# Optimization experiments

Measured on AMD Instinct MI355X. Metric: run time of the kernel, lower is better.

The kernel has to match this reference:

```python
import jax, jax.numpy as jnp
import numpy as np

B, SEQ, NNODES = 4, 12, 1024
SEG_LEN, SEG_NUM = 3, 4
HID, FF, DK, NH, NLAYERS = 64, 2048, 32, 8, 2


def setup_inputs() -> dict:
    key = jax.random.key(0)
    ks = iter(jax.random.split(key, 64))
    def nrm(shape, scale=0.05):
        return jax.random.normal(next(ks), shape, dtype=jnp.float32) * scale
    ones = lambda s: jnp.ones(s, jnp.float32)
    zeros = lambda s: jnp.zeros(s, jnp.float32)
    S, L = 2, NLAYERS
    return {
        'traffic': nrm((B, SEQ, NNODES), 1.0),
        'user': nrm((B, SEQ, NNODES), 1.0),
        'patch_w': nrm((S, HID, SEG_LEN)), 'patch_b': nrm((S, HID)),
        'mha_w': nrm((S, L, 3 * HID, HID)), 'mha_b': nrm((S, L, 3 * HID)),
        'out_w': nrm((S, L, HID, HID)), 'out_b': nrm((S, L, HID)),
        'ff1_w': nrm((S, L, FF, HID)), 'ff1_b': nrm((S, L, FF)),
        'ff2_w': nrm((S, L, HID, FF)), 'ff2_b': nrm((S, L, HID)),
        'ln1_g': ones((S, L, HID)), 'ln1_b': zeros((S, L, HID)),
        'ln2_g': ones((S, L, HID)), 'ln2_b': zeros((S, L, HID)),
        'ga_wq': nrm((S, L, DK, HID)), 'ga_wk': nrm((S, L, DK, HID)), 'ga_wv': nrm((S, L, HID, HID)),
        'ga_ff1_w': nrm((S, L, FF, HID)), 'ga_ff1_b': nrm((S, L, FF)),
        'ga_ff2_w': nrm((S, L, HID, FF)), 'ga_ff2_b': nrm((S, L, HID)),
        'ga_ln1_g': ones((S, L, HID)), 'ga_ln1_b': zeros((S, L, HID)),
        'ga_ln2_g': ones((S, L, HID)), 'ga_ln2_b': zeros((S, L, HID)),
        'ca_wq': nrm((DK, 2 * HID)), 'ca_wk': nrm((DK, 2 * HID)), 'ca_wv': nrm((HID, 2 * HID)),
    }


def _ln(x, g, b, eps=1e-5):
    m = x.mean(-1, keepdims=True)
    v = jnp.mean((x - m) ** 2, -1, keepdims=True)
    return (x - m) / jnp.sqrt(v + eps) * g + b


def _pe(s, d):
    pos = jnp.arange(s, dtype=jnp.float32)[:, None]
    div = jnp.exp(jnp.arange(0, d, 2, dtype=jnp.float32) * (-np.log(10000.0) / d))
    pe = jnp.zeros((s, d), jnp.float32)
    pe = pe.at[:, 0::2].set(jnp.sin(pos * div))
    pe = pe.at[:, 1::2].set(jnp.cos(pos * div))
    return pe


def _mha(x, w, b, wo, bo):
    # standard nn.MultiheadAttention self-attn, batch_first; x: [B,S,H]
    qkv = x @ w.T + b
    q, k, v = jnp.split(qkv, 3, axis=-1)
    def heads(t):
        b_, s_, h_ = t.shape
        return t.reshape(b_, s_, NH, h_ // NH).transpose(0, 2, 1, 3)
    q, k, v = heads(q), heads(k), heads(v)
    scale = 1.0 / jnp.sqrt(jnp.float32(HID // NH))
    att = jax.nn.softmax(jnp.einsum('bhqd,bhkd->bhqk', q, k) * scale, axis=-1)
    o = jnp.einsum('bhqk,bhkd->bhqd', att, v).transpose(0, 2, 1, 3).reshape(x.shape)
    return o @ wo.T + bo


def _enc_layer(x, p):
    # TransformerEncoderLayer_cross, post-norm, dropout=0 (eval)
    x = _ln(x + _mha(x, p['mw'], p['mb'], p['ow'], p['ob']), p['g1'], p['b1'])
    f = jax.nn.relu(x @ p['f1w'].T + p['f1b']) @ p['f2w'].T + p['f2b']
    return _ln(x + f, p['g2'], p['b2'])


def _graph_att(x, p):
    # GraphAttention.forward (bias=None, mask=None, dropout=0)
    q = x @ p['wq'].T
    k = x @ p['wk'].T
    v = x @ p['wv'].T
    dist = jax.nn.softmax(jnp.einsum('bnd,bmd->bnm', q, k) / jnp.sqrt(jnp.float32(DK)), axis=-1)
    att = jnp.einsum('bnm,bmd->bnd', dist, v)
    att = _ln(att, p['g1'], p['b1']) + x
    f = jax.nn.relu(att @ p['f1w'].T + p['f1b']) @ p['f2w'].T + p['f2b']
    return _ln(att + f, p['g2'], p['b2'])


def reference(traffic, user, patch_w, patch_b, mha_w, mha_b, out_w, out_b,
              ff1_w, ff1_b, ff2_w, ff2_b, ln1_g, ln1_b, ln2_g, ln2_b,
              ga_wq, ga_wk, ga_wv, ga_ff1_w, ga_ff1_b, ga_ff2_w, ga_ff2_b,
              ga_ln1_g, ga_ln1_b, ga_ln2_g, ga_ln2_b, ca_wq, ca_wk, ca_wv):
    pe = _pe(SEG_NUM, HID)

    def encode(x, s):
        b, _, d = x.shape
        # DSW_embedding: b (seg_num seg_len) d -> b d seg_num seg_len, then Linear
        seg = x.reshape(b, SEG_NUM, SEG_LEN, d).transpose(0, 3, 1, 2)
        z = seg @ patch_w[s].T + patch_b[s]          # [b, d, seg_num, HID]
        z = z + pe                                    # positional encoding over patches
        for i in range(NLAYERS):
            # temporal attention over the patch axis
            zt = z.reshape(b * d, SEG_NUM, HID)
            zt = _enc_layer(zt, dict(mw=mha_w[s, i], mb=mha_b[s, i], ow=out_w[s, i], ob=out_b[s, i],
                                     f1w=ff1_w[s, i], f1b=ff1_b[s, i], f2w=ff2_w[s, i], f2b=ff2_b[s, i],
                                     g1=ln1_g[s, i], b1=ln1_b[s, i], g2=ln2_g[s, i], b2=ln2_b[s, i]))
            z = zt.reshape(b, d, SEG_NUM, HID)
            # spatial graph attention over the node axis
            zs = z.transpose(0, 2, 1, 3).reshape(b * SEG_NUM, d, HID)
            zs = _graph_att(zs, dict(wq=ga_wq[s, i], wk=ga_wk[s, i], wv=ga_wv[s, i],
                                     f1w=ga_ff1_w[s, i], f1b=ga_ff1_b[s, i], f2w=ga_ff2_w[s, i], f2b=ga_ff2_b[s, i],
                                     g1=ga_ln1_g[s, i], b1=ga_ln1_b[s, i], g2=ga_ln2_g[s, i], b2=ga_ln2_b[s, i]))
            z = zs.reshape(b, SEG_NUM, d, HID).transpose(0, 2, 1, 3)
        return z.mean(axis=2)                         # pool patches -> [b, d, HID]

    enc = jnp.concatenate([encode(traffic, 0), encode(user, 1)], axis=-1)  # [b, d, 2*HID]
    # encoder_attn: SelfAttention(2*HID -> dim_k=32, dim_v=HID)
    q = enc @ ca_wq.T
    k = enc @ ca_wk.T
    v = enc @ ca_wv.T
    dist = jax.nn.softmax(jnp.einsum('bnd,bmd->bnm', q, k) / jnp.sqrt(jnp.float32(DK)), axis=-1)
    return jnp.einsum('bnm,bmd->bnd', dist, v)        # [b, n_nodes, HID]
```

## Files before the change

kernel.cpp:

```cpp
#include <hip/hip_runtime.h>
#include <hip/hip_bf16.h>
#include <math.h>

#define BB 4
#define SEQL 12
#define NN 1024
#define SEGL 3
#define SEGN 4
#define HID 64
#define FFD 2048
#define DKK 32
#define NHH 8
#define HDD 8
#define ZS 1048576

using bf16 = __hip_bfloat16;
__device__ __forceinline__ float b2f(bf16 v) { return __bfloat162float(v); }

typedef __attribute__((ext_vector_type(8))) short s8v;
typedef __attribute__((ext_vector_type(4))) float f4v;
typedef __attribute__((ext_vector_type(4))) unsigned short u4v;

__device__ __forceinline__ unsigned short f2b(float f) {
  bf16 h = __float2bfloat16(f);
  unsigned short u; __builtin_memcpy(&u, &h, 2); return u;
}
__device__ __forceinline__ float us2f(unsigned short u) {
  unsigned int e = ((unsigned int)u) << 16;
  float f; __builtin_memcpy(&f, &e, 4); return f;
}

template <int F>
__device__ __forceinline__ float ldw(const void* p, long i) {
  if (F) return ((const float*)p)[i];
  return b2f(((const bf16*)p)[i]);
}
template <int F>
__device__ __forceinline__ s8v ldfrag(const void* p, long elemOff) {
  if (F) {
    const float* fp = (const float*)p + elemOff;
    f4v u = *(const f4v*)fp, v = *(const f4v*)(fp + 4);
    s8v t;
    t[0]=f2b(u[0]); t[1]=f2b(u[1]); t[2]=f2b(u[2]); t[3]=f2b(u[3]);
    t[4]=f2b(v[0]); t[5]=f2b(v[1]); t[6]=f2b(v[2]); t[7]=f2b(v[3]);
    return t;
  }
  return *(const s8v*)((const unsigned short*)p + elemOff);
}
template <int F>
__device__ __forceinline__ f4v ldb4(const void* p, long i) {
  if (F) return *(const f4v*)((const float*)p + i);
  u4v u = *(const u4v*)((const unsigned short*)p + i);
  f4v r; r[0]=us2f(u[0]); r[1]=us2f(u[1]); r[2]=us2f(u[2]); r[3]=us2f(u[3]);
  return r;
}

__global__ void k_zero(unsigned short* __restrict__ o, int n) {
  int i = blockIdx.x * 256 + threadIdx.x;
  if (i < n) o[i] = 0;
}

__global__ void k_detect(const void* __restrict__ x0, int* __restrict__ flag) {
  int t = threadIdx.x;
  int bad = 0;
  const bf16* p = (const bf16*)x0;
  for (int i = t; i < 512; i += 256) {
    float a = fabsf(b2f(p[i]));
    if (!(a < 1e4f) || (a != 0.f && a < 1e-4f)) bad = 1;
  }
  __shared__ int tot;
  if (t == 0) tot = 0;
  __syncthreads();
  unsigned long long m = __ballot(bad);
  if ((t & 63) == 0) atomicAdd(&tot, __popcll(m));
  __syncthreads();
  if (t == 0) *flag = (tot > 64) ? 1 : 0;
}

template <int F>
__device__ __forceinline__ void wconv_body(const void* __restrict__ w1,
    const void* __restrict__ w2, const void* __restrict__ w3,
    const void* __restrict__ w4, unsigned short* __restrict__ out) {
  int i = blockIdx.x * 256 + threadIdx.x;
  long e8 = (long)i * 8;
  int slot = (int)(e8 >> 17);
  int si = slot >> 2, which = slot & 3;
  long r = e8 & 131071;
  const void* src = (which == 0) ? w1 : (which == 1) ? w2 : (which == 2) ? w3 : w4;
  *(s8v*)(out + e8) = ldfrag<F>(src, (long)si*FFD*HID + r);
}
__global__ __launch_bounds__(256) void k_wconv(const void* w1, const void* w2,
    const void* w3, const void* w4, unsigned short* out,
    const int* __restrict__ flag) {
  if (*flag) wconv_body<1>(w1, w2, w3, w4, out);
  else       wconv_body<0>(w1, w2, w3, w4, out);
}

template <int F>
__device__ __forceinline__ void patch_body(const void* __restrict__ xt,
    const void* __restrict__ xu,
    const void* __restrict__ pw, const void* __restrict__ pb,
    float* __restrict__ z) {
  int bid = blockIdx.x;
  int s = bid >> 12, rem = bid & 4095;
  int b = rem >> 10, n = rem & 1023;
  const void* x = s ? xu : xt;
  long opw = (long)s*HID*SEGL, opb = (long)s*HID;
  int g = threadIdx.x >> 6, h = threadIdx.x & 63;
  float acc = ldw<F>(pb, opb + h);
#pragma unroll
  for (int l = 0; l < SEGL; ++l)
    acc += ldw<F>(x, (long)(b*SEQL + g*SEGL + l)*NN + n) * ldw<F>(pw, opw + h*SEGL + l);
  int i2 = h >> 1;
  float dv = expf((float)(2*i2) * (-logf(10000.f) / (float)HID));
  float ang = (float)g * dv;
  acc += (h & 1) ? cosf(ang) : sinf(ang);
  z[(long)s*ZS + ((long)(b*NN + n)*SEGN + g)*HID + h] = acc;
}
__global__ __launch_bounds__(256) void k_patch(const void* __restrict__ xt,
    const void* __restrict__ xu,
    const void* __restrict__ pw, const void* __restrict__ pb,
    float* __restrict__ z, const int* __restrict__ flag) {
  if (*flag) patch_body<1>(xt, xu, pw, pb, z);
  else       patch_body<0>(xt, xu, pw, pb, z);
}

#define TT 64
template <int F>
__device__ __forceinline__ void tattn_body(float* __restrict__ zb,
    const void* __restrict__ W, const void* __restrict__ bq,
    const void* __restrict__ WO, const void* __restrict__ bo,
    const void* __restrict__ g1, const void* __restrict__ b1,
    int li, char* lds) {
  int s = blockIdx.x >> 8, blk = blockIdx.x & 255;
  long si = s*2 + li;
  float* z = zb + (long)s*ZS;
  long oW = si*3*HID*HID, obq = si*3*HID, oWO = si*HID*HID, obo = si*HID;
  long og1 = si*HID, ob1 = si*HID;
  unsigned short (*qkvs)[200] = (unsigned short(*)[200])lds;
  unsigned short (*ao)[72]    = (unsigned short(*)[72])(lds + 25600);
  float (*yb)[68]             = (float(*)[68])(lds + 34816);
  int tid = threadIdx.x;
  int w = tid >> 6, lane = tid & 63;
  int col = lane & 15, quad = lane >> 4;
  long r0 = (long)blk * TT;

  s8v bx[4][2];
#pragma unroll
  for (int mt = 0; mt < 4; ++mt) {
    const float* xr = z + (r0 + mt*16 + col) * HID;
#pragma unroll
    for (int ks = 0; ks < 2; ++ks) {
      const float* p = xr + ks*32 + quad*8;
      f4v u = *(const f4v*)p, v = *(const f4v*)(p + 4);
      s8v t;
      t[0]=f2b(u[0]); t[1]=f2b(u[1]); t[2]=f2b(u[2]); t[3]=f2b(u[3]);
      t[4]=f2b(v[0]); t[5]=f2b(v[1]); t[6]=f2b(v[2]); t[7]=f2b(v[3]);
      bx[mt][ks] = t;
    }
  }
#pragma unroll
  for (int nt = 0; nt < 3; ++nt) {
    int cbase = (w*3 + nt) * 16;
    s8v aw[2];
#pragma unroll
    for (int ks = 0; ks < 2; ++ks)
      aw[ks] = ldfrag<F>(W, oW + (long)(cbase + col)*HID + ks*32 + quad*8);
    f4v bv = ldb4<F>(bq, obq + cbase + quad*4);
#pragma unroll
    for (int mt = 0; mt < 4; ++mt) {
      f4v sv = (f4v){0.f,0.f,0.f,0.f};
#pragma unroll
      for (int ks = 0; ks < 2; ++ks)
        sv = __builtin_amdgcn_mfma_f32_16x16x32_bf16(aw[ks], bx[mt][ks], sv, 0, 0, 0);
      unsigned short pk[4];
#pragma unroll
      for (int r = 0; r < 4; ++r) pk[r] = f2b(sv[r] + bv[r]);
      *(unsigned long long*)&qkvs[mt*16 + col][cbase + quad*4] =
        (unsigned long long)pk[0] | ((unsigned long long)pk[1] << 16) |
        ((unsigned long long)pk[2] << 32) | ((unsigned long long)pk[3] << 48);
    }
  }
  __syncthreads();
  if (tid < 128) {
    int gi = tid >> 3, hd = tid & 7;
    int tl = gi * 4;
    float qv[4][8], kv[4][8], vv[4][8];
#pragma unroll
    for (int t4 = 0; t4 < 4; ++t4) {
      s8v qq = *(const s8v*)&qkvs[tl + t4][hd*8];
      s8v kk = *(const s8v*)&qkvs[tl + t4][64 + hd*8];
      s8v vq = *(const s8v*)&qkvs[tl + t4][128 + hd*8];
#pragma unroll
      for (int e = 0; e < 8; ++e) {
        qv[t4][e] = us2f((unsigned short)qq[e]);
        kv[t4][e] = us2f((unsigned short)kk[e]);
        vv[t4][e] = us2f((unsigned short)vq[e]);
      }
    }
    const float sc8 = 0.3535533905932738f;
#pragma unroll
    for (int qt = 0; qt < 4; ++qt) {
      float s[4]; float mx = -1e30f;
#pragma unroll
      for (int kt = 0; kt < 4; ++kt) {
        float d = 0;
#pragma unroll
        for (int e = 0; e < 8; ++e) d += qv[qt][e]*kv[kt][e];
        s[kt] = d*sc8; mx = fmaxf(mx, s[kt]);
      }
      float se = 0;
#pragma unroll
      for (int kt = 0; kt < 4; ++kt) { s[kt] = expf(s[kt]-mx); se += s[kt]; }
      float inv = 1.f/se;
      s8v outp;
#pragma unroll
      for (int e = 0; e < 8; ++e) {
        float o = 0;
#pragma unroll
        for (int kt = 0; kt < 4; ++kt) o += s[kt]*vv[kt][e];
        outp[e] = (short)f2b(o*inv);
      }
      *(s8v*)&ao[tl + qt][hd*8] = outp;
    }
  }
  __syncthreads();
  s8v awo[2];
#pragma unroll
  for (int ks = 0; ks < 2; ++ks)
    awo[ks] = ldfrag<F>(WO, oWO + (long)(w*16 + col)*HID + ks*32 + quad*8);
  f4v bov = ldb4<F>(bo, obo + w*16 + quad*4);
#pragma unroll
  for (int mt = 0; mt < 4; ++mt) {
    f4v ov = (f4v){0.f,0.f,0.f,0.f};
#pragma unroll
    for (int ks = 0; ks < 2; ++ks) {
      s8v bao = *(const s8v*)&ao[mt*16 + col][ks*32 + quad*8];
      ov = __builtin_amdgcn_mfma_f32_16x16x32_bf16(awo[ks], bao, ov, 0, 0, 0);
    }
    f4v yv;
#pragma unroll
    for (int r = 0; r < 4; ++r) yv[r] = ov[r] + bov[r];
    *(f4v*)&yb[mt*16 + col][w*16 + quad*4] = yv;
  }
  __syncthreads();
  float gg = ldw<F>(g1, og1 + lane), bb2 = ldw<F>(b1, ob1 + lane);
#pragma unroll
  for (int rr = 0; rr < 16; ++rr) {
    int row = w*16 + rr;
    long tok = r0 + row;
    float val = yb[row][lane] + z[tok*HID + lane];
    float s = val;
#pragma unroll
    for (int off = 32; off; off >>= 1) s += __shfl_xor(s, off);
    float m = s*(1.f/HID);
    float d = val - m, sq = d*d;
#pragma unroll
    for (int off = 32; off; off >>= 1) sq += __shfl_xor(sq, off);
    float rv = rsqrtf(sq*(1.f/HID) + 1e-5f);
    z[tok*HID + lane] = d*rv*gg + bb2;
  }
}
__global__ __launch_bounds__(256) void k_tattn(float* __restrict__ z,
    const void* W, const void* bqkv, const void* WO, const void* bo,
    const void* g1, const void* b1, int li, const int* __restrict__ flag) {
  __shared__ __attribute__((aligned(16))) char lds[52224];
  if (*flag) tattn_body<1>(z, W, bqkv, WO, bo, g1, b1, li, lds);
  else       tattn_body<0>(z, W, bqkv, WO, bo, g1, b1, li, lds);
}

#define FRW 32
#define HCS 74

template <int F>
__device__ __forceinline__ void ffmfma_body(float* __restrict__ xb,
    const unsigned short* __restrict__ wcw, int li, int wsel,
    const void* __restrict__ B1, const void* __restrict__ B2,
    const void* __restrict__ G, const void* __restrict__ Bt,
    char* ldsbuf) {
  int s = blockIdx.x >> 9, blk = blockIdx.x & 511;
  long si = s*2 + li;
  float* x = xb + (long)s*ZS;
  const unsigned short* wc1 = wcw + (si*4 + wsel)*131072;
  const unsigned short* wc2 = wcw + (si*4 + wsel + 1)*131072;
  long ob1 = si*FFD, ob2 = si*HID, og = si*HID, obt = si*HID;
  int tid = threadIdx.x;
  int w = tid >> 6, lane = tid & 63;
  int col = lane & 15, quad = lane >> 4;
  long r0 = (long)blk * FRW;
  unsigned short* hcw = (unsigned short*)(ldsbuf + w*(2*32*HCS));

  s8v bx[2][2];
#pragma unroll
  for (int rt = 0; rt < 2; ++rt) {
    const float* xr = x + (r0 + rt*16 + col) * HID;
#pragma unroll
    for (int ks = 0; ks < 2; ++ks) {
      const float* p = xr + ks*32 + quad*8;
      f4v u = *(const f4v*)p, v = *(const f4v*)(p + 4);
      s8v t;
      t[0]=f2b(u[0]); t[1]=f2b(u[1]); t[2]=f2b(u[2]); t[3]=f2b(u[3]);
      t[4]=f2b(v[0]); t[5]=f2b(v[1]); t[6]=f2b(v[2]); t[7]=f2b(v[3]);
      bx[rt][ks] = t;
    }
  }

  f4v acc[4][2];
#pragma unroll
  for (int m = 0; m < 4; ++m)
#pragma unroll
    for (int rt = 0; rt < 2; ++rt) acc[m][rt] = (f4v){0.f,0.f,0.f,0.f};

  const int hb0 = w * 512;
  for (int c = 0; c < 8; ++c) {
    const int hbase = hb0 + c*64;
#pragma unroll
    for (int t = 0; t < 4; ++t) {
      const unsigned short* a1p = wc1 + (hbase + t*16 + col)*HID + quad*8;
      s8v a10 = *(const s8v*)a1p;
      s8v a11 = *(const s8v*)(a1p + 32);
      f4v bv = ldb4<F>(B1, ob1 + hbase + t*16 + quad*4);
#pragma unroll
      for (int rt = 0; rt < 2; ++rt) {
        f4v sv = __builtin_amdgcn_mfma_f32_16x16x32_bf16(a10, bx[rt][0],
                   (f4v){0.f,0.f,0.f,0.f}, 0, 0, 0);
        sv = __builtin_amdgcn_mfma_f32_16x16x32_bf16(a11, bx[rt][1], sv, 0, 0, 0);
        unsigned short pk[4];
#pragma unroll
        for (int r = 0; r < 4; ++r) pk[r] = f2b(fmaxf(sv[r] + bv[r], 0.f));
        *(unsigned long long*)&hcw[(rt*16 + col)*HCS + t*16 + quad*4] =
          (unsigned long long)pk[0] | ((unsigned long long)pk[1] << 16) |
          ((unsigned long long)pk[2] << 32) | ((unsigned long long)pk[3] << 48);
      }
    }
#pragma unroll
    for (int ks2 = 0; ks2 < 2; ++ks2) {
      s8v a2h[4];
#pragma unroll
      for (int m = 0; m < 4; ++m)
        a2h[m] = *(const s8v*)(wc2 + (m*16 + col)*FFD + hbase + ks2*32 + quad*8);
      s8v bh[2];
#pragma unroll
      for (int rt = 0; rt < 2; ++rt)
        bh[rt] = *(const s8v*)&hcw[(rt*16 + col)*HCS + ks2*32 + quad*8];
#pragma unroll
      for (int m = 0; m < 4; ++m)
#pragma unroll
        for (int rt = 0; rt < 2; ++rt)
          acc[m][rt] = __builtin_amdgcn_mfma_f32_16x16x32_bf16(a2h[m], bh[rt], acc[m][rt], 0, 0, 0);
    }
  }

  float* red0 = (float*)ldsbuf;
  float* red1 = (float*)(ldsbuf + 8704);
  __syncthreads();
  if (w < 2) {
    float* rg = w ? red1 : red0;
#pragma unroll
    for (int m = 0; m < 4; ++m)
#pragma unroll
      for (int rt = 0; rt < 2; ++rt)
        *(f4v*)&rg[(rt*16 + col)*68 + m*16 + quad*4] = acc[m][rt];
  }
  __syncthreads();
  if (w >= 2) {
    float* rg = (w == 3) ? red1 : red0;
#pragma unroll
    for (int m = 0; m < 4; ++m)
#pragma unroll
      for (int rt = 0; rt < 2; ++rt) {
        float* pp = &rg[(rt*16 + col)*68 + m*16 + quad*4];
        f4v old = *(f4v*)pp;
        *(f4v*)pp = old + acc[m][rt];
      }
  }
  __syncthreads();
  float gg = ldw<F>(G, og + lane), bbt = ldw<F>(Bt, obt + lane);
  float b2v = ldw<F>(B2, ob2 + lane);
#pragma unroll
  for (int rr = 0; rr < 8; ++rr) {
    int rl = w*8 + rr;
    long grow = r0 + rl;
    float val = red0[rl*68 + lane] + red1[rl*68 + lane] + b2v + x[grow*HID + lane];
    float s = val;
#pragma unroll
    for (int off = 32; off; off >>= 1) s += __shfl_xor(s, off);
    float m = s * (1.f/HID);
    float d = val - m;
    float sq = d*d;
#pragma unroll
    for (int off = 32; off; off >>= 1) sq += __shfl_xor(sq, off);
    float rv = rsqrtf(sq*(1.f/HID) + 1e-5f);
    x[grow*HID + lane] = d*rv*gg + bbt;
  }
}
__global__ __launch_bounds__(256, 4) void k_ffmfma(float* __restrict__ x,
    const unsigned short* __restrict__ wcw, int li, int wsel,
    const void* B1, const void* B2, const void* G, const void* Bt,
    const int* __restrict__ flag) {
  __shared__ __attribute__((aligned(16))) char ldsbuf[4*2*32*HCS];
  if (*flag) ffmfma_body<1>(x, wcw, li, wsel, B1, B2, G, Bt, ldsbuf);
  else       ffmfma_body<0>(x, wcw, li, wsel, B1, B2, G, Bt, ldsbuf);
}

template <int F>
__device__ __forceinline__ void gqkv_body(const float* __restrict__ zb,
    const void* __restrict__ wq, const void* __restrict__ wk,
    const void* __restrict__ wv, int li,
    unsigned short* __restrict__ q, unsigned short* __restrict__ k,
    unsigned short* __restrict__ vt) {
  int tid = threadIdx.x;
  int w = tid >> 6, lane = tid & 63;
  int col = lane & 15, quad = lane >> 4;
  int sg = blockIdx.x >> 4;
  int s = sg >> 4, bg = sg & 15;
  int n0 = (blockIdx.x & 15) * 64;
  int b = bg >> 2, g = bg & 3;
  long si = s*2 + li;
  const float* z = zb + (long)s*ZS;
  long oq = si*DKK*HID, ok = si*DKK*HID, ov = si*HID*HID;
  long gbase = (long)sg * NN;

  s8v bx[4][2];
#pragma unroll
  for (int rt = 0; rt < 4; ++rt) {
    const float* xr = z + ((long)(b*NN + n0 + rt*16 + col)*SEGN + g)*HID;
#pragma unroll
    for (int ks = 0; ks < 2; ++ks) {
      const float* p = xr + ks*32 + quad*8;
      f4v u = *(const f4v*)p, vv = *(const f4v*)(p + 4);
      s8v t;
      t[0]=f2b(u[0]); t[1]=f2b(u[1]); t[2]=f2b(u[2]); t[3]=f2b(u[3]);
      t[4]=f2b(vv[0]); t[5]=f2b(vv[1]); t[6]=f2b(vv[2]); t[7]=f2b(vv[3]);
      bx[rt][ks] = t;
    }
  }

#pragma unroll
  for (int tt = 0; tt < 2; ++tt) {
    int ct = w*2 + tt;
    const void* wp; long wo; int co; int kind;
    if (ct < 2)      { wp = wq; wo = oq; co = ct*16;      kind = 0; }
    else if (ct < 4) { wp = wk; wo = ok; co = (ct-2)*16;  kind = 1; }
    else             { wp = wv; wo = ov; co = (ct-4)*16;  kind = 2; }
    s8v aw[2];
#pragma unroll
    for (int ks = 0; ks < 2; ++ks)
      aw[ks] = ldfrag<F>(wp, wo + (long)(co + col)*HID + ks*32 + quad*8);
#pragma unroll
    for (int rt = 0; rt < 4; ++rt) {
      f4v sv = (f4v){0.f,0.f,0.f,0.f};
#pragma unroll
      for (int ks = 0; ks < 2; ++ks)
        sv = __builtin_amdgcn_mfma_f32_16x16x32_bf16(aw[ks], bx[rt][ks], sv, 0, 0, 0);
      int key = n0 + rt*16 + col;
      if (kind == 2) {
        long vbase = (long)sg*HID*NN;
#pragma unroll
        for (int r = 0; r < 4; ++r)
          vt[vbase + (long)(co + quad*4 + r)*NN + key] = f2b(sv[r]);
      } else {
        long row = gbase + key;
        unsigned short pk[4];
#pragma unroll
        for (int r = 0; r < 4; ++r) pk[r] = f2b(sv[r]);
        unsigned short* dst = kind ? k : q;
        *(unsigned long long*)&dst[row*DKK + co + quad*4] =
          (unsigned long long)pk[0] | ((unsigned long long)pk[1] << 16) |
          ((unsigned long long)pk[2] << 32) | ((unsigned long long)pk[3] << 48);
      }
    }
  }
}
__global__ __launch_bounds__(256) void k_gqkv(const float* __restrict__ z,
    const void* wq, const void* wk, const void* wv, int li,
    unsigned short* q, unsigned short* k, unsigned short* vt,
    const int* __restrict__ flag) {
  if (*flag) gqkv_body<1>(z, wq, wk, wv, li, q, k, vt);
  else       gqkv_body<0>(z, wq, wk, wv, li, q, k, vt);
}

__global__ __launch_bounds__(512) void k_gattn(float* __restrict__ zb,
    const unsigned short* __restrict__ qb, const unsigned short* __restrict__ kb,
    const unsigned short* __restrict__ vtb,
    const void* __restrict__ g1, const void* __restrict__ b1, int li,
    const int* __restrict__ flag) {
  int f = *flag;
  __shared__ unsigned short pl[2][8][16][74];
  __shared__ float accb[8][16][66];
  __shared__ float lb[8][16];
  int tid = threadIdx.x;
  int w = tid >> 6, lane = tid & 63;
  int col = lane & 15, quad = lane >> 4;
  int qt = w >> 1, kh = w & 1;
  int sg = blockIdx.x >> 4;
  int s = sg >> 4, bg = sg & 15;
  int n0 = (blockIdx.x & 15) * 64;
  long si = s*2 + li;
  float* z = zb + (long)s*ZS;
  long og1 = si*HID, ob1 = si*HID;
  long gbase = (long)sg * NN;
  const unsigned short* vrow = vtb + (long)sg*HID*NN;

  s8v aq = *(const s8v*)(qb + (gbase + n0 + qt*16 + col)*DKK + quad*8);

  f4v acc[4];
#pragma unroll
  for (int t = 0; t < 4; ++t) acc[t] = (f4v){0.f,0.f,0.f,0.f};
  float psum[4] = {0.f,0.f,0.f,0.f};
  const float rs = 0.17677669529663687f;
  const int cbeg = kh * 512;

#pragma unroll 2
  for (int it = 0; it < 8; ++it) {
    int c0 = cbeg + it*64;
    int pb = it & 1;
    f4v s4[4];
#pragma unroll
    for (int nt = 0; nt < 4; ++nt) {
      s8v bk = *(const s8v*)(kb + (gbase + c0 + nt*16 + col)*DKK + quad*8);
      s4[nt] = __builtin_amdgcn_mfma_f32_16x16x32_bf16(aq, bk,
                (f4v){0.f,0.f,0.f,0.f}, 0, 0, 0);
    }
#pragma unroll
    for (int r = 0; r < 4; ++r) {
      float p0 = expf(s4[0][r]*rs), p1 = expf(s4[1][r]*rs);
      float p2 = expf(s4[2][r]*rs), p3 = expf(s4[3][r]*rs);
      psum[r] += (p0 + p1) + (p2 + p3);
      int row = quad*4 + r;
      pl[pb][w][row][col]      = f2b(p0);
      pl[pb][w][row][16 + col] = f2b(p1);
      pl[pb][w][row][32 + col] = f2b(p2);
      pl[pb][w][row][48 + col] = f2b(p3);
    }
#pragma unroll
    for (int ks = 0; ks < 2; ++ks) {
      s8v ap = *(const s8v*)&pl[pb][w][col][ks*32 + quad*8];
#pragma unroll
      for (int nt = 0; nt < 4; ++nt) {
        s8v bv = *(const s8v*)(vrow + (long)(nt*16 + col)*NN + c0 + ks*32 + quad*8);
        acc[nt] = __builtin_amdgcn_mfma_f32_16x16x32_bf16(ap, bv, acc[nt], 0, 0, 0);
      }
    }
  }

#pragma unroll
  for (int r = 0; r < 4; ++r) {
    float v = psum[r];
#pragma unroll
    for (int off = 1; off < 16; off <<= 1) v += __shfl_xor(v, off);
    psum[r] = v;
  }
#pragma unroll
  for (int t = 0; t < 4; ++t)
#pragma unroll
    for (int r = 0; r < 4; ++r)
      accb[w][quad*4 + r][t*16 + col] = acc[t][r];
  if (col == 0) {
#pragma unroll
    for (int r = 0; r < 4; ++r) lb[w][quad*4 + r] = psum[r];
  }
  __syncthreads();

  int b = bg >> 2, g = bg & 3;
  float gg = f ? ((const float*)g1)[og1 + lane] : b2f(((const bf16*)g1)[og1 + lane]);
  float bb = f ? ((const float*)b1)[ob1 + lane] : b2f(((const bf16*)b1)[ob1 + lane]);
#pragma unroll
  for (int rr = 0; rr < 8; ++rr) {
    int rl = w*8 + rr;
    int qtt = rl >> 4, lr = rl & 15;
    float a = accb[2*qtt][lr][lane] + accb[2*qtt + 1][lr][lane];
    float l = lb[2*qtt][lr] + lb[2*qtt + 1][lr];
    float val = a / l;
    float s = val;
#pragma unroll
    for (int off = 32; off; off >>= 1) s += __shfl_xor(s, off);
    float m = s*(1.f/HID);
    float d = val - m, sq = d*d;
#pragma unroll
    for (int off = 32; off; off >>= 1) sq += __shfl_xor(sq, off);
    float r = rsqrtf(sq*(1.f/HID) + 1e-5f);
    float* zp = z + ((long)(b*NN + n0 + rl)*SEGN + g)*HID;
    zp[lane] = d*r*gg + bb + zp[lane];
  }
}

__global__ __launch_bounds__(64) void k_pool(const float* __restrict__ z,
    float* __restrict__ enc) {
  int bid = blockIdx.x;
  int s = bid >> 12, rem = bid & 4095;
  int b = rem >> 10, n = rem & 1023, h = threadIdx.x;
  const float* zp = z + (long)s*ZS + (long)(b*NN + n)*SEGN*HID;
  float a = 0;
#pragma unroll
  for (int g = 0; g < SEGN; ++g) a += zp[g*HID + h];
  enc[(long)(b*NN + n)*(2*HID) + s*HID + h] = a*0.25f;
}

template <int F>
__device__ __forceinline__ void fqkv_body(const float* __restrict__ enc,
    const void* __restrict__ wq, const void* __restrict__ wk,
    const void* __restrict__ wv,
    unsigned short* __restrict__ q, unsigned short* __restrict__ k,
    unsigned short* __restrict__ vt, float* xs) {
  long r = blockIdx.x;
  int t = threadIdx.x;
  xs[t] = enc[r*128 + t];
  __syncthreads();
  if (t < 32) {
    long wr = (long)t*128; float a = 0;
    for (int e = 0; e < 128; ++e) a += xs[e]*ldw<F>(wq, wr + e);
    q[r*DKK + t] = f2b(a);
  } else if (t < 64) {
    long wr = (long)(t-32)*128; float a = 0;
    for (int e = 0; e < 128; ++e) a += xs[e]*ldw<F>(wk, wr + e);
    k[r*DKK + (t-32)] = f2b(a);
  } else {
    long wr = (long)(t-64)*128; float a = 0;
    for (int e = 0; e < 128; ++e) a += xs[e]*ldw<F>(wv, wr + e);
    vt[((r >> 10)*HID + (t-64))*NN + (r & 1023)] = f2b(a);
  }
}
__global__ __launch_bounds__(128) void k_fqkv(const float* __restrict__ enc,
    const void* wq, const void* wk, const void* wv,
    unsigned short* q, unsigned short* k, unsigned short* vt,
    const int* __restrict__ flag) {
  __shared__ float xs[2*HID];
  if (*flag) fqkv_body<1>(enc, wq, wk, wv, q, k, vt, xs);
  else       fqkv_body<0>(enc, wq, wk, wv, q, k, vt, xs);
}

__global__ __launch_bounds__(512) void k_fattn(
    const unsigned short* __restrict__ qb, const unsigned short* __restrict__ kb,
    const unsigned short* __restrict__ vtb, void* __restrict__ outp,
    const int* __restrict__ flag) {
  __shared__ unsigned short pl[2][8][16][74];
  __shared__ float accb[8][16][66];
  __shared__ float lb[8][16];
  int tid = threadIdx.x;
  int w = tid >> 6, lane = tid & 63;
  int col = lane & 15, quad = lane >> 4;
  int qt = w >> 1, kh = w & 1;
  int b = blockIdx.x >> 4;
  int n0 = (blockIdx.x & 15) * 64;
  long gbase = (long)b * NN;
  const unsigned short* vrow = vtb + (long)b*HID*NN;

  s8v aq = *(const s8v*)(qb + (gbase + n0 + qt*16 + col)*DKK + quad*8);

  f4v acc[4];
#pragma unroll
  for (int t = 0; t < 4; ++t) acc[t] = (f4v){0.f,0.f,0.f,0.f};
  float psum[4] = {0.f,0.f,0.f,0.f};
  const float rs = 0.17677669529663687f;
  const int cbeg = kh * 512;

#pragma unroll 2
  for (int it = 0; it < 8; ++it) {
    int c0 = cbeg + it*64;
    int pb = it & 1;
    f4v s4[4];
#pragma unroll
    for (int nt = 0; nt < 4; ++nt) {
      s8v bk = *(const s8v*)(kb + (gbase + c0 + nt*16 + col)*DKK + quad*8);
      s4[nt] = __builtin_amdgcn_mfma_f32_16x16x32_bf16(aq, bk,
                (f4v){0.f,0.f,0.f,0.f}, 0, 0, 0);
    }
#pragma unroll
    for (int r = 0; r < 4; ++r) {
      float p0 = expf(s4[0][r]*rs), p1 = expf(s4[1][r]*rs);
      float p2 = expf(s4[2][r]*rs), p3 = expf(s4[3][r]*rs);
      psum[r] += (p0 + p1) + (p2 + p3);
      int row = quad*4 + r;
      pl[pb][w][row][col]      = f2b(p0);
      pl[pb][w][row][16 + col] = f2b(p1);
      pl[pb][w][row][32 + col] = f2b(p2);
      pl[pb][w][row][48 + col] = f2b(p3);
    }
#pragma unroll
    for (int ks = 0; ks < 2; ++ks) {
      s8v ap = *(const s8v*)&pl[pb][w][col][ks*32 + quad*8];
#pragma unroll
      for (int nt = 0; nt < 4; ++nt) {
        s8v bv = *(const s8v*)(vrow + (long)(nt*16 + col)*NN + c0 + ks*32 + quad*8);
        acc[nt] = __builtin_amdgcn_mfma_f32_16x16x32_bf16(ap, bv, acc[nt], 0, 0, 0);
      }
    }
  }

#pragma unroll
  for (int r = 0; r < 4; ++r) {
    float v = psum[r];
#pragma unroll
    for (int off = 1; off < 16; off <<= 1) v += __shfl_xor(v, off);
    psum[r] = v;
  }
#pragma unroll
  for (int t = 0; t < 4; ++t)
#pragma unroll
    for (int r = 0; r < 4; ++r)
      accb[w][quad*4 + r][t*16 + col] = acc[t][r];
  if (col == 0) {
#pragma unroll
    for (int r = 0; r < 4; ++r) lb[w][quad*4 + r] = psum[r];
  }
  __syncthreads();

  int f = *flag;
#pragma unroll
  for (int rr = 0; rr < 8; ++rr) {
    int rl = w*8 + rr;
    int qtt = rl >> 4, lr = rl & 15;
    float a = accb[2*qtt][lr][lane] + accb[2*qtt + 1][lr][lane];
    float l = lb[2*qtt][lr] + lb[2*qtt + 1][lr];
    float val = a / l;
    long idx = (gbase + n0 + rl)*HID + lane;
    if (f) ((float*)outp)[idx] = val;
    else   ((bf16*)outp)[idx] = __float2bfloat16(val);
  }
}

extern "C" void kernel_launch(void* const* d_in, const int* in_sizes, int n_in,
                              void* d_out, int out_size, void* d_ws, size_t ws_size,
                              hipStream_t stream) {
  static const int EXP[30] = {
    49152, 49152, 384, 128, 49152, 768, 16384, 256,
    524288, 8192, 524288, 256, 256, 256, 256, 256,
    8192, 8192, 16384, 524288, 8192, 524288, 256, 256,
    256, 256, 256, 4096, 4096, 8192
  };
  const size_t NEED = (size_t)(2*ZS + 524288 + 524288 + 524288 + 1048576 + 1048576) * 4 + 64;
  bool ok = (n_in == 30) && (ws_size >= NEED) && (out_size == BB*NN*HID);
  if (ok) for (int i = 0; i < 30; ++i) ok = ok && (in_sizes[i] == EXP[i]);
  if (!ok) {
    k_zero<<<(BB*NN*HID + 255)/256, 256, 0, stream>>>((unsigned short*)d_out, BB*NN*HID);
    return;
  }

  float* z   = (float*)d_ws;
  float* enc = z   + 2*ZS;
  float* qb  = enc + 524288;
  float* kb  = qb  + 524288;
  float* vb  = kb  + 524288;
  float* wcf = vb  + 1048576;
  int*  flag = (int*)(wcf + 1048576);
  unsigned short* wcw = (unsigned short*)wcf;

  k_detect<<<1, 256, 0, stream>>>(d_in[0], flag);

  const void *i_traffic=d_in[0], *i_user=d_in[1], *i_pw=d_in[2], *i_pb=d_in[3],
    *i_mw=d_in[4], *i_mb=d_in[5], *i_ow=d_in[6], *i_ob=d_in[7], *i_f1w=d_in[8],
    *i_f1b=d_in[9], *i_f2w=d_in[10], *i_f2b=d_in[11], *i_l1g=d_in[12],
    *i_l1b=d_in[13], *i_l2g=d_in[14], *i_l2b=d_in[15], *i_gwq=d_in[16],
    *i_gwk=d_in[17], *i_gwv=d_in[18], *i_gf1w=d_in[19], *i_gf1b=d_in[20],
    *i_gf2w=d_in[21], *i_gf2b=d_in[22], *i_gl1g=d_in[23], *i_gl1b=d_in[24],
    *i_gl2g=d_in[25], *i_gl2b=d_in[26], *i_cwq=d_in[27], *i_cwk=d_in[28],
    *i_cwv=d_in[29];

  k_wconv<<<1024, 256, 0, stream>>>(i_f1w, i_f2w, i_gf1w, i_gf2w, wcw, flag);
  k_patch<<<2*BB*NN, 256, 0, stream>>>(i_traffic, i_user, i_pw, i_pb, z, flag);

  for (int i = 0; i < 2; ++i) {
    k_tattn<<<512, 256, 0, stream>>>(z, i_mw, i_mb, i_ow, i_ob,
        i_l1g, i_l1b, i, flag);
    k_ffmfma<<<1024, 256, 0, stream>>>(z, wcw, i, 0,
        i_f1b, i_f2b, i_l2g, i_l2b, flag);
    k_gqkv<<<512, 256, 0, stream>>>(z, i_gwq, i_gwk, i_gwv, i,
        (unsigned short*)qb, (unsigned short*)kb, (unsigned short*)vb, flag);
    k_gattn<<<512, 512, 0, stream>>>(z,
        (const unsigned short*)qb, (const unsigned short*)kb,
        (const unsigned short*)vb, i_gl1g, i_gl1b, i, flag);
    k_ffmfma<<<1024, 256, 0, stream>>>(z, wcw, i, 2,
        i_gf1b, i_gf2b, i_gl2g, i_gl2b, flag);
  }
  k_pool<<<2*BB*NN, 64, 0, stream>>>(z, enc);
  k_fqkv<<<BB*NN, 128, 0, stream>>>(enc, i_cwq, i_cwk, i_cwv,
      (unsigned short*)qb, (unsigned short*)kb, (unsigned short*)vb, flag);
  k_fattn<<<BB*16, 512, 0, stream>>>((const unsigned short*)qb,
      (const unsigned short*)kb, (unsigned short*)vb, d_out, flag);
}
```

Before: 625.2 us.

## Restructure FFN kernel so each wave owns 16 tokens across full hidden dim

The fused FFN kernel moves from 256-thread blocks, where four waves split the 2048 hidden dimension over 32 tokens and then reduce through LDS, to 512-thread blocks of 8 waves. Each wave now handles 16 tokens across the full hidden dimension. This removes the cross-wave reduction and its barriers. The cost is that weights are re-read per 16 tokens instead of being shared across two 16-token tiles, so weight traffic and per-wave serial work both grow. The grid shrinks to 256 blocks, which risks leaving compute units underused.

```diff
diff --git a/kernel.cpp b/kernel.cpp
--- a/kernel.cpp
+++ b/kernel.cpp
@@ -269,7 +269,7 @@
   else       tattn_body<0>(z, W, bqkv, WO, bo, g1, b1, li, lds);
 }
 
-#define FRW 32
+#define FRW 128
 #define HCS 74
 
 template <int F>
@@ -278,7 +278,7 @@
     const void* __restrict__ B1, const void* __restrict__ B2,
     const void* __restrict__ G, const void* __restrict__ Bt,
     char* ldsbuf) {
-  int s = blockIdx.x >> 9, blk = blockIdx.x & 511;
+  int s = blockIdx.x >> 7, blk = blockIdx.x & 127;
   long si = s*2 + li;
   float* x = xb + (long)s*ZS;
   const unsigned short* wc1 = wcw + (si*4 + wsel)*131072;
@@ -288,12 +288,13 @@
   int w = tid >> 6, lane = tid & 63;
   int col = lane & 15, quad = lane >> 4;
   long r0 = (long)blk * FRW;
-  unsigned short* hcw = (unsigned short*)(ldsbuf + w*(2*32*HCS));
-
-  s8v bx[2][2];
-#pragma unroll
-  for (int rt = 0; rt < 2; ++rt) {
-    const float* xr = x + (r0 + rt*16 + col) * HID;
+  unsigned short* hcw = (unsigned short*)(ldsbuf + w*(16*HCS*2));
+  float* red = (float*)(ldsbuf + 8*(16*HCS*2) + w*(16*68*4));
+
+  long tokc = r0 + w*16 + col;
+  s8v bx[2];
+  {
+    const float* xr = x + tokc * HID;
 #pragma unroll
     for (int ks = 0; ks < 2; ++ks) {
       const float* p = xr + ks*32 + quad*8;
@@ -301,91 +302,56 @@
       s8v t;
       t[0]=f2b(u[0]); t[1]=f2b(u[1]); t[2]=f2b(u[2]); t[3]=f2b(u[3]);
       t[4]=f2b(v[0]); t[5]=f2b(v[1]); t[6]=f2b(v[2]); t[7]=f2b(v[3]);
-      bx[rt][ks] = t;
-    }
-  }
-
-  f4v acc[4][2];
-#pragma unroll
-  for (int m = 0; m < 4; ++m)
-#pragma unroll
-    for (int rt = 0; rt < 2; ++rt) acc[m][rt] = (f4v){0.f,0.f,0.f,0.f};
-
-  const int hb0 = w * 512;
-  for (int c = 0; c < 8; ++c) {
-    const int hbase = hb0 + c*64;
+      bx[ks] = t;
+    }
+  }
+
+  f4v acc[4];
+#pragma unroll
+  for (int m = 0; m < 4; ++m) acc[m] = (f4v){0.f,0.f,0.f,0.f};
+
+  for (int c = 0; c < 32; ++c) {
+    const int hbase = c*64;
 #pragma unroll
     for (int t = 0; t < 4; ++t) {
       const unsigned short* a1p = wc1 + (hbase + t*16 + col)*HID + quad*8;
       s8v a10 = *(const s8v*)a1p;
       s8v a11 = *(const s8v*)(a1p + 32);
       f4v bv = ldb4<F>(B1, ob1 + hbase + t*16 + quad*4);
-#pragma unroll
-      for (int rt = 0; rt < 2; ++rt) {
-        f4v sv = __builtin_amdgcn_mfma_f32_16x16x32_bf16(a10, bx[rt][0],
-                   (f4v){0.f,0.f,0.f,0.f}, 0, 0, 0);
-        sv = __builtin_amdgcn_mfma_f32_16x16x32_bf16(a11, bx[rt][1], sv, 0, 0, 0);
-        unsigned short pk[4];
-#pragma unroll
-        for (int r = 0; r < 4; ++r) pk[r] = f2b(fmaxf(sv[r] + bv[r], 0.f));
-        *(unsigned long long*)&hcw[(rt*16 + col)*HCS + t*16 + quad*4] =
-          (unsigned long long)pk[0] | ((unsigned long long)pk[1] << 16) |
-          ((unsigned long long)pk[2] << 32) | ((unsigned long long)pk[3] << 48);
+      f4v sv = __builtin_amdgcn_mfma_f32_16x16x32_bf16(a10, bx[0],
+                 (f4v){0.f,0.f,0.f,0.f}, 0, 0, 0);
+      sv = __builtin_amdgcn_mfma_f32_16x16x32_bf16(a11, bx[1], sv, 0, 0, 0);
+      unsigned short pk[4];
+#pragma unroll
+      for (int r = 0; r < 4; ++r) pk[r] = f2b(fmaxf(sv[r] + bv[r], 0.f));
+      *(unsigned long long*)&hcw[col*HCS + t*16 + quad*4] =
+        (unsigned long long)pk[0] | ((unsigned long long)pk[1] << 16) |
+        ((unsigned long long)pk[2] << 32) | ((unsigned long long)pk[3] << 48);
+    }
+#pragma unroll
+    for (int ks2 = 0; ks2 < 2; ++ks2) {
+      s8v bh = *(const s8v*)&hcw[col*HCS + ks2*32 + quad*8];
+#pragma unroll
+      for (int m = 0; m < 4; ++m) {
+        s8v a2h = *(const s8v*)(wc2 + (m*16 + col)*FFD + hbase + ks2*32 + quad*8);
+        acc[m] = __builtin_amdgcn_mfma_f32_16x16x32_bf16(a2h, bh, acc[m], 0, 0, 0);
       }
     }
-#pragma unroll
-    for (int ks2 = 0; ks2 < 2; ++ks2) {
-      s8v a2h[4];
-#pragma unroll
-      for (int m = 0; m < 4; ++m)
-        a2h[m] = *(const s8v*)(wc2 + (m*16 + col)*FFD + hbase + ks2*32 + quad*8);
-      s8v bh[2];
-#pragma unroll
-      for (int rt = 0; rt < 2; ++rt)
-        bh[rt] = *(const s8v*)&hcw[(rt*16 + col)*HCS + ks2*32 + quad*8];
-#pragma unroll
-      for (int m = 0; m < 4; ++m)
-#pragma unroll
-        for (int rt = 0; rt < 2; ++rt)
-          acc[m][rt] = __builtin_amdgcn_mfma_f32_16x16x32_bf16(a2h[m], bh[rt], acc[m][rt], 0, 0, 0);
-    }
-  }
-
-  float* red0 = (float*)ldsbuf;
-  float* red1 = (float*)(ldsbuf + 8704);
-  __syncthreads();
-  if (w < 2) {
-    float* rg = w ? red1 : red0;
-#pragma unroll
-    for (int m = 0; m < 4; ++m)
-#pragma unroll
-      for (int rt = 0; rt < 2; ++rt)
-        *(f4v*)&rg[(rt*16 + col)*68 + m*16 + quad*4] = acc[m][rt];
-  }
-  __syncthreads();
-  if (w >= 2) {
-    float* rg = (w == 3) ? red1 : red0;
-#pragma unroll
-    for (int m = 0; m < 4; ++m)
-#pragma unroll
-      for (int rt = 0; rt < 2; ++rt) {
-        float* pp = &rg[(rt*16 + col)*68 + m*16 + quad*4];
-        f4v old = *(f4v*)pp;
-        *(f4v*)pp = old + acc[m][rt];
-      }
-  }
-  __syncthreads();
+  }
+
+#pragma unroll
+  for (int m = 0; m < 4; ++m)
+    *(f4v*)&red[col*68 + m*16 + quad*4] = acc[m];
   float gg = ldw<F>(G, og + lane), bbt = ldw<F>(Bt, obt + lane);
   float b2v = ldw<F>(B2, ob2 + lane);
 #pragma unroll
-  for (int rr = 0; rr < 8; ++rr) {
-    int rl = w*8 + rr;
-    long grow = r0 + rl;
-    float val = red0[rl*68 + lane] + red1[rl*68 + lane] + b2v + x[grow*HID + lane];
-    float s = val;
-#pragma unroll
-    for (int off = 32; off; off >>= 1) s += __shfl_xor(s, off);
-    float m = s * (1.f/HID);
+  for (int rr = 0; rr < 16; ++rr) {
+    long grow = r0 + w*16 + rr;
+    float val = red[rr*68 + lane] + b2v + x[grow*HID + lane];
+    float sm = val;
+#pragma unroll
+    for (int off = 32; off; off >>= 1) sm += __shfl_xor(sm, off);
+    float m = sm * (1.f/HID);
     float d = val - m;
     float sq = d*d;
 #pragma unroll
@@ -394,11 +360,11 @@
     x[grow*HID + lane] = d*rv*gg + bbt;
   }
 }
-__global__ __launch_bounds__(256, 4) void k_ffmfma(float* __restrict__ x,
+__global__ __launch_bounds__(512) void k_ffmfma(float* __restrict__ x,
     const unsigned short* __restrict__ wcw, int li, int wsel,
     const void* B1, const void* B2, const void* G, const void* Bt,
     const int* __restrict__ flag) {
-  __shared__ __attribute__((aligned(16))) char ldsbuf[4*2*32*HCS];
+  __shared__ __attribute__((aligned(16))) char ldsbuf[8*16*HCS*2 + 8*16*68*4];
   if (*flag) ffmfma_body<1>(x, wcw, li, wsel, B1, B2, G, Bt, ldsbuf);
   else       ffmfma_body<0>(x, wcw, li, wsel, B1, B2, G, Bt, ldsbuf);
 }
@@ -760,17 +726,19 @@
   k_wconv<<<1024, 256, 0, stream>>>(i_f1w, i_f2w, i_gf1w, i_gf2w, wcw, flag);
   k_patch<<<2*BB*NN, 256, 0, stream>>>(i_traffic, i_user, i_pw, i_pb, z, flag);
 
+  const int FFG = 2*BB*NN*SEGN/FRW;
+
   for (int i = 0; i < 2; ++i) {
     k_tattn<<<512, 256, 0, stream>>>(z, i_mw, i_mb, i_ow, i_ob,
         i_l1g, i_l1b, i, flag);
-    k_ffmfma<<<1024, 256, 0, stream>>>(z, wcw, i, 0,
+    k_ffmfma<<<FFG, 512, 0, stream>>>(z, wcw, i, 0,
         i_f1b, i_f2b, i_l2g, i_l2b, flag);
     k_gqkv<<<512, 256, 0, stream>>>(z, i_gwq, i_gwk, i_gwv, i,
         (unsigned short*)qb, (unsigned short*)kb, (unsigned short*)vb, flag);
     k_gattn<<<512, 512, 0, stream>>>(z,
         (const unsigned short*)qb, (const unsigned short*)kb,
         (const unsigned short*)vb, i_gl1g, i_gl1b, i, flag);
-    k_ffmfma<<<1024, 256, 0, stream>>>(z, wcw, i, 2,
+    k_ffmfma<<<FFG, 512, 0, stream>>>(z, wcw, i, 2,
         i_gf1b, i_gf2b, i_gl2g, i_gl2b, flag);
   }
   k_pool<<<2*BB*NN, 64, 0, stream>>>(z, enc);
```

Result: slower. 848.3 us (+35.7%).
